# Optimization experiments

Measured on AMD Instinct MI355X. Metric: run time of the kernel, lower is better.

## Reference

```python
import jax, jax.numpy as jnp
import numpy as np
from jax import lax

K_NEIGH = 10


def setup_inputs() -> dict:
    key = jax.random.key(0)
    k1, k2, k3, k4, k5 = jax.random.split(key, 5)
    bs, C, T = 8, 256, 2048
    x = jax.random.normal(k1, (bs, C, T), dtype=jnp.float32)
    num_frms = jax.random.randint(k2, (bs,), 0, 2048)
    # Conv1d(in=C, out=C, kernel=3, pad=1): weight [out, in, k], bias [out]
    conv_w = jax.random.normal(k3, (C, C, 3), dtype=jnp.float32) * (1.0 / np.sqrt(3 * C))
    conv_b = jnp.zeros((C,), dtype=jnp.float32)
    # Linear(2*C -> C): weight [out, 2*in], bias [out]
    mlp_w = jax.random.normal(k4, (C, 2 * C), dtype=jnp.float32) * (1.0 / np.sqrt(2 * C))
    mlp_b = jax.random.normal(k5, (C,), dtype=jnp.float32) * 0.01
    return {"x": x, "num_frms": num_frms, "conv_w": conv_w, "conv_b": conv_b,
            "mlp_w": mlp_w, "mlp_b": mlp_b}


def _knn_idx(x, k):
    # x: [bs, C, T]; dif[b,i,j] = ||x[b,:,i] - x[b,:,j]||^2 via norm expansion
    sq = jnp.sum(x * x, axis=1)                      # [bs, T]
    gram = jnp.einsum('bci,bcj->bij', x, x)          # [bs, T, T]
    dif = sq[:, :, None] + sq[:, None, :] - 2.0 * gram
    _, idx = lax.top_k(-dif, k)                      # k smallest distances
    return idx                                       # [bs, T, k]


def reference(x, num_frms, conv_w, conv_b, mlp_w, mlp_b):
    bs, C, T = x.shape
    Cout = conv_w.shape[0]
    # temporal conv branch (kernel 3, stride 1, pad 1)
    c_out = lax.conv_general_dilated(
        x, conv_w, window_strides=(1,), padding=((1, 1),),
        dimension_numbers=('NCH', 'OIH', 'NCH')) + conv_b[None, :, None]
    # graph branch ('par': knn on x)
    idx = _knn_idx(x, K_NEIGH)                                   # [bs, T, k]
    idx_flat = (idx + jnp.arange(bs)[:, None, None] * T).reshape(-1, K_NEIGH)
    feat = x.transpose(0, 2, 1).reshape(bs * T, C)               # [N, C]
    feat_neigh = feat[idx_flat]                                  # [N, k, C]
    ctr = feat[:, None, :]                                       # [N, 1, C]
    cat = jnp.concatenate(
        [feat_neigh, jnp.broadcast_to(ctr, feat_neigh.shape)], axis=-1)  # [N,k,2C]
    g = jnp.einsum('nkc,oc->nko', cat, mlp_w) + mlp_b            # [N, k, Cout]
    # cosine edge weight
    num = jnp.einsum('nkc,nc->nk', feat_neigh, feat)
    den = jnp.sqrt(jnp.sum(feat_neigh * feat_neigh, axis=2)) * \
          jnp.sqrt(jnp.sum(feat * feat, axis=1))[:, None]
    w = num / den                                                # [N, k]
    g = g * w[:, :, None]
    g = jnp.max(g, axis=1)                                       # [N, Cout]
    g_out = g.reshape(bs, T, Cout).transpose(0, 2, 1)            # [bs, Cout, T]
    out = jax.nn.relu(c_out + g_out)
    # MaxPool1d(kernel=2, stride=2)
    out = out.reshape(bs, Cout, T // 2, 2).max(axis=-1)
    return out
```

## Files before the change

kernel.cpp:

```cpp
#include <hip/hip_runtime.h>
#include <hip/hip_bf16.h>
#include <cstdint>

#define T_DIM 2048
#define C_DIM 256
#define BS 8
#define NPTS (BS * T_DIM)
#define KNB 10
#define NCH 16

typedef __bf16 bf16x8 __attribute__((ext_vector_type(8)));
typedef float f32x4 __attribute__((ext_vector_type(4)));
typedef unsigned long long u64;

#define AS1 __attribute__((address_space(1)))
#define AS3 __attribute__((address_space(3)))

__device__ __forceinline__ unsigned short f2bf_rn(float f) {
  unsigned u = __float_as_uint(f);
  unsigned r = (u + 0x7FFFu + ((u >> 16) & 1u)) >> 16;
  return (unsigned short)r;
}
__device__ __forceinline__ float bfbits2f(unsigned short h) {
  return __uint_as_float((unsigned)h << 16);
}
__device__ __forceinline__ __bf16 bfbits(unsigned short h) {
  return __builtin_bit_cast(__bf16, h);
}

__device__ __forceinline__ unsigned key_hi(float sqi, float sqj, float gv) {
  float dif = __fmaf_rn(-2.0f, gv, __fadd_rn(sqi, sqj));
  unsigned u = __float_as_uint(dif);
  return (u & 0x80000000u) ? ~u : (u | 0x80000000u);
}
__device__ __forceinline__ unsigned flip32(float dif) {
  unsigned u = __float_as_uint(dif);
  return (u & 0x80000000u) ? ~u : (u | 0x80000000u);
}

__device__ __forceinline__ void stage_tile(const __bf16* __restrict__ src, size_t row0,
                                           int ld, int k0, __bf16* lds, int w, int l) {
  int kofs = ((l & 7) ^ (l >> 3)) * 8;
  const __bf16* g0 = src + (row0 + (size_t)(l >> 3)) * ld + k0 + kofs;
  __bf16* lbase = lds + (size_t)(w * 4) * 512;
#pragma unroll
  for (int q4 = 0; q4 < 4; ++q4) {
    __builtin_amdgcn_global_load_lds((AS1 void*)(g0 + (size_t)(w * 4 + q4) * 8 * ld),
                                     (AS3 void*)(lbase + q4 * 512), 16, 0, 0);
  }
}

__device__ __forceinline__ void stage_tile_conv(const __bf16* __restrict__ src, int m0,
                                                int k0in, const __bf16* __restrict__ zp,
                                                __bf16* lds, int w, int l) {
  int tap = k0in >> 8;
  int kshift = tap - 1;
  int k0 = k0in & 255;
  int kofs = ((l & 7) ^ (l >> 3)) * 8;
  int mb = m0 & (T_DIM - 1);
#pragma unroll
  for (int q4 = 0; q4 < 4; ++q4) {
    int q = w * 4 + q4;
    int row = q * 8 + (l >> 3);
    int t = mb + row + kshift;
    const __bf16* g = ((unsigned)t < (unsigned)T_DIM)
                          ? (src + (size_t)(m0 + row + kshift) * C_DIM + k0 + kofs)
                          : (zp + kofs);
    __builtin_amdgcn_global_load_lds((AS1 void*)g, (AS3 void*)(lds + q * 512), 16, 0, 0);
  }
}

__device__ __forceinline__ bf16x8 read_frag(const __bf16* lds, int t16, int ks, int l) {
  int row = t16 * 16 + (l & 15);
  int kb = ks * 64 + ((l >> 4) << 4);
  int byte = row * 128 + (kb ^ ((row & 7) << 4));
  return *(const bf16x8*)((const char*)lds + byte);
}

__global__ __launch_bounds__(256) void k_transpose_split(const float* __restrict__ x,
                                                         __bf16* __restrict__ Fh,
                                                         __bf16* __restrict__ Fl) {
  __shared__ float tile[32][33];
  int b = blockIdx.z;
  int t0 = blockIdx.x * 32;
  int c0 = blockIdx.y * 32;
  int tx = threadIdx.x & 31, ty = threadIdx.x >> 5;
  const float* xb = x + (size_t)b * C_DIM * T_DIM;
#pragma unroll
  for (int r = 0; r < 4; ++r) {
    int c = c0 + ty + 8 * r;
    tile[ty + 8 * r][tx] = xb[(size_t)c * T_DIM + t0 + tx];
  }
  __syncthreads();
#pragma unroll
  for (int r = 0; r < 4; ++r) {
    int t = t0 + ty + 8 * r;
    float v = tile[tx][ty + 8 * r];
    unsigned short hb = f2bf_rn(v);
    float lo = v - bfbits2f(hb);
    size_t o = ((size_t)b * T_DIM + t) * C_DIM + c0 + tx;
    Fh[o] = bfbits(hb);
    Fl[o] = bfbits(f2bf_rn(lo));
  }
}

__global__ __launch_bounds__(256) void k_sq(const __bf16* __restrict__ Fh,
                                            const __bf16* __restrict__ Fl,
                                            float* __restrict__ sq) {
  int n = blockIdx.x * 4 + (threadIdx.x >> 6);
  int lane = threadIdx.x & 63;
  ushort4 hv = ((const ushort4*)Fh)[(size_t)n * 64 + lane];
  ushort4 lv = ((const ushort4*)Fl)[(size_t)n * 64 + lane];
  float s = 0.f;
  {
    float v;
    v = bfbits2f(hv.x) + bfbits2f(lv.x); s = fmaf(v, v, s);
    v = bfbits2f(hv.y) + bfbits2f(lv.y); s = fmaf(v, v, s);
    v = bfbits2f(hv.z) + bfbits2f(lv.z); s = fmaf(v, v, s);
    v = bfbits2f(hv.w) + bfbits2f(lv.w); s = fmaf(v, v, s);
  }
#pragma unroll
  for (int d = 1; d < 64; d <<= 1) s += __shfl_xor(s, d, 64);
  if (lane == 0) sq[n] = s;
}

__global__ __launch_bounds__(256) void k_gram_reduce(const __bf16* __restrict__ Fh,
                                                     const __bf16* __restrict__ Fl,
                                                     const float* __restrict__ sq,
                                                     u64* __restrict__ kbuf,
                                                     u64* __restrict__ bbuf) {
  __shared__ __bf16 Bh[128 * 64], Bl[128 * 64];
  __shared__ float sqc[128];

  int ch = blockIdx.x, p = blockIdx.y, b = blockIdx.z;
  size_t base = (size_t)b * T_DIM;
  const float* sqb = sq + base;
  int tid = threadIdx.x, w = tid >> 6, l = tid & 63, g = l >> 4;
  int r0 = p * 64;
  int cand0 = ch * 128;
  int myrow = r0 + w * 16 + (l & 15);
  float sqi = sqb[myrow];
  if (tid < 128) sqc[tid] = sqb[cand0 + tid];

  const __bf16* rowbaseh = Fh + ((size_t)(base + myrow)) * C_DIM + g * 8;
  const __bf16* rowbasel = Fl + ((size_t)(base + myrow)) * C_DIM + g * 8;

  f32x4 acc[8];
#pragma unroll
  for (int j = 0; j < 8; ++j) acc[j] = {0.f, 0.f, 0.f, 0.f};

  for (int k0 = 0; k0 < C_DIM; k0 += 64) {
    stage_tile(Fh, base + cand0, C_DIM, k0, Bh, w, l);
    stage_tile(Fl, base + cand0, C_DIM, k0, Bl, w, l);
    bf16x8 rhf0 = *(const bf16x8*)(rowbaseh + k0);
    bf16x8 rhf1 = *(const bf16x8*)(rowbaseh + k0 + 32);
    bf16x8 rlf0 = *(const bf16x8*)(rowbasel + k0);
    bf16x8 rlf1 = *(const bf16x8*)(rowbasel + k0 + 32);
    __syncthreads();
#pragma unroll
    for (int ks = 0; ks < 2; ++ks) {
      bf16x8 rh = ks ? rhf1 : rhf0;
      bf16x8 rl = ks ? rlf1 : rlf0;
      bf16x8 cv[8];
#pragma unroll
      for (int j = 0; j < 8; ++j) cv[j] = read_frag(Bh, j, ks, l);
#pragma unroll
      for (int j = 0; j < 8; ++j)
        acc[j] = __builtin_amdgcn_mfma_f32_16x16x32_bf16(cv[j], rh, acc[j], 0, 0, 0);
#pragma unroll
      for (int j = 0; j < 8; ++j)
        acc[j] = __builtin_amdgcn_mfma_f32_16x16x32_bf16(cv[j], rl, acc[j], 0, 0, 0);
#pragma unroll
      for (int j = 0; j < 8; ++j) cv[j] = read_frag(Bl, j, ks, l);
#pragma unroll
      for (int j = 0; j < 8; ++j)
        acc[j] = __builtin_amdgcn_mfma_f32_16x16x32_bf16(cv[j], rh, acc[j], 0, 0, 0);
    }
    __syncthreads();
  }

  u64 c0 = ~0ull, c1 = ~0ull, c2 = ~0ull, c3 = ~0ull;
#pragma unroll
  for (int j = 0; j < 8; ++j) {
    f32x4 sv = *(const f32x4*)&sqc[j * 16 + (g << 2)];
#pragma unroll
    for (int r = 0; r < 4; ++r) {
      unsigned u = key_hi(sqi, sv[r], acc[j][r]);
      u64 key = ((u64)u << 32) | (unsigned)(cand0 + j * 16 + (g << 2) + r);
      u64 t1 = (key > c0) ? key : c0; c0 = (key < c0) ? key : c0;
      u64 t2 = (t1 > c1) ? t1 : c1;  c1 = (t1 < c1) ? t1 : c1;
      u64 t3 = (t2 > c2) ? t2 : c2;  c2 = (t2 < c2) ? t2 : c2;
      c3 = (t3 < c3) ? t3 : c3;
    }
  }
  u64* kp = kbuf + ((((size_t)b * NCH + ch) * T_DIM + myrow) * 12 + g * 3);
  kp[0] = c0;
  kp[1] = c1;
  kp[2] = c2;
  u64 bd = c3;
  { u64 o = __shfl_xor(bd, 16, 64); bd = (o < bd) ? o : bd; }
  { u64 o = __shfl_xor(bd, 32, 64); bd = (o < bd) ? o : bd; }
  if (g == 0) bbuf[((size_t)b * NCH + ch) * T_DIM + myrow] = bd;
}

__global__ __launch_bounds__(256) void k_topk_merge(const u64* __restrict__ kbuf,
                                                    const u64* __restrict__ bbuf,
                                                    const float* __restrict__ sq,
                                                    int* __restrict__ idxo,
                                                    float* __restrict__ wo,
                                                    int* __restrict__ fixlist,
                                                    int* __restrict__ fixcount) {
  int b = blockIdx.y;
  int row = blockIdx.x * 4 + (threadIdx.x >> 6);
  int lane = threadIdx.x & 63;
  const float* sqb = sq + (size_t)b * T_DIM;
  float sqi = sqb[row];

  const u64* kp = kbuf + ((((size_t)b * NCH + (lane >> 2)) * T_DIM + row) * 12 + (lane & 3) * 3);
  u64 m0 = kp[0], m1 = kp[1], m2 = kp[2];
  u64 excl = (lane < NCH) ? bbuf[((size_t)b * NCH + lane) * T_DIM + row] : ~0ull;

  u64 win[KNB];
#pragma unroll
  for (int s = 0; s < KNB; ++s) {
    unsigned mh = (unsigned)(m0 >> 32);
    unsigned h = mh;
#pragma unroll
    for (int d = 1; d < 64; d <<= 1) {
      unsigned oh = __shfl_xor(h, d, 64);
      h = (oh < h) ? oh : h;
    }
    unsigned lo = (mh == h) ? (unsigned)m0 : 0xFFFFFFFFu;
#pragma unroll
    for (int d = 1; d < 64; d <<= 1) {
      unsigned ol = __shfl_xor(lo, d, 64);
      lo = (ol < lo) ? ol : lo;
    }
    u64 m = ((u64)h << 32) | lo;
    win[s] = m;
    bool pop = (m0 == m);
    m0 = pop ? m1 : m0;
    m1 = pop ? m2 : m1;
    m2 = pop ? ~0ull : m2;
  }
  u64 theta = win[KNB - 1];

  u64 mywin = win[0];
#pragma unroll
  for (int s = 1; s < KNB; ++s) mywin = (lane == s) ? win[s] : mywin;
  if (lane < KNB) {
    int j = (int)(unsigned)(mywin & 0xffffffffull);
    unsigned su = (unsigned)(mywin >> 32);
    unsigned bits = (su & 0x80000000u) ? (su & 0x7fffffffu) : ~su;
    float dif = __uint_as_float(bits);
    float sqj = sqb[j];
    float num = 0.5f * (sqi + sqj - dif);
    float wv = num / (sqrtf(sqi) * sqrtf(sqj));
    idxo[((size_t)b * T_DIM + row) * KNB + lane] = j;
    wo[((size_t)b * T_DIM + row) * KNB + lane] = wv;
  }

#pragma unroll
  for (int d = 1; d < 64; d <<= 1) {
    u64 o = __shfl_xor(excl, d, 64);
    excl = (o < excl) ? o : excl;
  }
  if (lane == 0 && excl < theta) {
    int slot = atomicAdd(fixcount, 1);
    fixlist[slot] = (int)(b * T_DIM + row);
  }
}

__global__ __launch_bounds__(256) void k_fix_dots(const __bf16* __restrict__ Fh,
                                                  const __bf16* __restrict__ Fl,
                                                  const float* __restrict__ sq,
                                                  const int* __restrict__ fixlist,
                                                  const int* __restrict__ fixcount,
                                                  u64* __restrict__ kpart) {
  __shared__ float xr[C_DIM];
  __shared__ float difs[64];
  int n = fixcount[0];
  int q = blockIdx.x;
  int tid = threadIdx.x;
  const unsigned short* fh = (const unsigned short*)Fh;
  const unsigned short* fl = (const unsigned short*)Fl;
  for (int i = blockIdx.y; i < n; i += gridDim.y) {
    int rowg = fixlist[i];
    int b = rowg >> 11, r = rowg & (T_DIM - 1);
    xr[tid] = bfbits2f(fh[(size_t)rowg * C_DIM + tid]) + bfbits2f(fl[(size_t)rowg * C_DIM + tid]);
    __syncthreads();
    const float* sqb = sq + (size_t)b * T_DIM;
    float sqi = sqb[r];
    int cand = q * 64 + (tid >> 2);
    int qd = tid & 3;
    size_t jo = ((size_t)b * T_DIM + cand) * C_DIM + qd * 64;
    float p = 0.f;
#pragma unroll 4
    for (int k = 0; k < 16; ++k) {
      ushort4 h4 = *(const ushort4*)(fh + jo + k * 4);
      ushort4 l4 = *(const ushort4*)(fl + jo + k * 4);
      int xb_ = qd * 64 + k * 4;
      p = fmaf(bfbits2f(h4.x) + bfbits2f(l4.x), xr[xb_ + 0], p);
      p = fmaf(bfbits2f(h4.y) + bfbits2f(l4.y), xr[xb_ + 1], p);
      p = fmaf(bfbits2f(h4.z) + bfbits2f(l4.z), xr[xb_ + 2], p);
      p = fmaf(bfbits2f(h4.w) + bfbits2f(l4.w), xr[xb_ + 3], p);
    }
    p += __shfl_xor(p, 1, 64);
    p += __shfl_xor(p, 2, 64);
    if (qd == 0) difs[tid >> 2] = __fmaf_rn(-2.0f, p, __fadd_rn(sqi, sqb[cand]));
    __syncthreads();
    if (tid < 64) {
      int lane = tid;
      u64 key = ((u64)flip32(difs[lane]) << 32) | (unsigned)(q * 64 + lane);
      u64 mywin = ~0ull;
#pragma unroll
      for (int s = 0; s < KNB; ++s) {
        u64 m = key;
#pragma unroll
        for (int d = 1; d < 64; d <<= 1) {
          u64 o = __shfl_xor(m, d, 64);
          m = (o < m) ? o : m;
        }
        if (key == m) key = ~0ull;
        mywin = (lane == s) ? m : mywin;
      }
      if (lane < KNB) kpart[((size_t)i * 32 + q) * KNB + lane] = mywin;
    }
    __syncthreads();
  }
}

__global__ __launch_bounds__(256) void k_fix_merge(const float* __restrict__ sq,
                                                   const int* __restrict__ fixlist,
                                                   const int* __restrict__ fixcount,
                                                   const u64* __restrict__ kpart,
                                                   int* __restrict__ idxo,
                                                   float* __restrict__ wo) {
  int n = fixcount[0];
  int w = threadIdx.x >> 6, lane = threadIdx.x & 63;
  for (int i = blockIdx.x * 4 + w; i < n; i += gridDim.x * 4) {
    int rowg = fixlist[i];
    int b = rowg >> 11, r = rowg & (T_DIM - 1);
    const float* sqb = sq + (size_t)b * T_DIM;
    float sqi = sqb[r];
    const u64* kp = kpart + (size_t)i * 320;
    u64 s0 = kp[lane], s1 = ~0ull, s2 = ~0ull, s3 = ~0ull, s4 = ~0ull;
#pragma unroll
    for (int t = 1; t < 5; ++t) {
      u64 k = kp[lane + 64 * t];
      u64 hi;
      hi = (k > s0) ? k : s0; s0 = (k < s0) ? k : s0; k = hi;
      hi = (k > s1) ? k : s1; s1 = (k < s1) ? k : s1; k = hi;
      hi = (k > s2) ? k : s2; s2 = (k < s2) ? k : s2; k = hi;
      hi = (k > s3) ? k : s3; s3 = (k < s3) ? k : s3; k = hi;
      s4 = (k < s4) ? k : s4;
    }
    u64 mywin = ~0ull;
#pragma unroll
    for (int s = 0; s < KNB; ++s) {
      u64 m = s0;
#pragma unroll
      for (int d = 1; d < 64; d <<= 1) {
        u64 o = __shfl_xor(m, d, 64);
        m = (o < m) ? o : m;
      }
      bool pop = (s0 == m);
      s0 = pop ? s1 : s0; s1 = pop ? s2 : s1; s2 = pop ? s3 : s2;
      s3 = pop ? s4 : s3; s4 = pop ? ~0ull : s4;
      mywin = (lane == s) ? m : mywin;
    }
    if (lane < KNB) {
      int j = (int)(unsigned)(mywin & 0xffffffffull);
      unsigned su = (unsigned)(mywin >> 32);
      unsigned bits = (su & 0x80000000u) ? (su & 0x7fffffffu) : ~su;
      float dif = __uint_as_float(bits);
      float sqj = sqb[j];
      float num = 0.5f * (sqi + sqj - dif);
      float wv = num / (sqrtf(sqi) * sqrtf(sqj));
      idxo[((size_t)b * T_DIM + r) * KNB + lane] = j;
      wo[((size_t)b * T_DIM + r) * KNB + lane] = wv;
    }
  }
}

__global__ __launch_bounds__(256, 2) void k_gemm_fused(const __bf16* __restrict__ Fh,
                                                       const __bf16* __restrict__ mlpB,
                                                       const __bf16* __restrict__ wk3,
                                                       float* __restrict__ mlpout,
                                                       float* __restrict__ convout,
                                                       const __bf16* __restrict__ zp) {
  __shared__ __bf16 As[128 * 64], Bs[128 * 64];
  int bx = blockIdx.x;
  const __bf16* Bm;
  float* C;
  int N, K, conv, n0;
  if (bx < 4) {
    Bm = mlpB; C = mlpout; N = 512; K = 256; conv = 0; n0 = bx * 128;
  } else {
    Bm = wk3; C = convout; N = 256; K = 768; conv = 1; n0 = (bx - 4) * 128;
  }
  int m0 = blockIdx.y * 128;
  int tid = threadIdx.x, w = tid >> 6, l = tid & 63;
  int wr = w >> 1, wc = w & 1;
  f32x4 acc[4][4];
#pragma unroll
  for (int i = 0; i < 4; ++i)
#pragma unroll
    for (int j = 0; j < 4; ++j) acc[i][j] = {0.f, 0.f, 0.f, 0.f};

  for (int k0 = 0; k0 < K; k0 += 64) {
    if (conv)
      stage_tile_conv(Fh, m0, k0, zp, As, w, l);
    else
      stage_tile(Fh, (size_t)m0, C_DIM, k0, As, w, l);
    stage_tile(Bm, (size_t)n0, K, k0, Bs, w, l);
    __syncthreads();
#pragma unroll
    for (int ks = 0; ks < 2; ++ks) {
      bf16x8 af[4], bf_[4];
#pragma unroll
      for (int i = 0; i < 4; ++i) af[i] = read_frag(As, wr * 4 + i, ks, l);
#pragma unroll
      for (int j = 0; j < 4; ++j) bf_[j] = read_frag(Bs, wc * 4 + j, ks, l);
#pragma unroll
      for (int i = 0; i < 4; ++i)
#pragma unroll
        for (int j = 0; j < 4; ++j)
          acc[i][j] = __builtin_amdgcn_mfma_f32_16x16x32_bf16(af[i], bf_[j], acc[i][j], 0, 0, 0);
    }
    __syncthreads();
  }
#pragma unroll
  for (int i = 0; i < 4; ++i) {
    int mrow = m0 + wr * 64 + i * 16 + ((l >> 4) << 2);
#pragma unroll
    for (int j = 0; j < 4; ++j) {
      int ncol = n0 + wc * 64 + j * 16 + (l & 15);
      float* cp = C + (size_t)mrow * N + ncol;
#pragma unroll
      for (int r = 0; r < 4; ++r) cp[(size_t)r * N] = acc[i][j][r];
    }
  }
}

__global__ __launch_bounds__(256) void k_gfinal(const float* __restrict__ mlpout,
                                                const float* __restrict__ mlp_b,
                                                const int* __restrict__ idxo,
                                                const float* __restrict__ wo,
                                                const float* __restrict__ convb,
                                                const float* __restrict__ cb,
                                                float* __restrict__ out) {
  __shared__ float tile[32][33];
  __shared__ int sj[64][KNB];
  __shared__ float sw[64][KNB];
  int b = blockIdx.z, c0 = blockIdx.y * 32, t20 = blockIdx.x * 32;
  int tid = threadIdx.x;
  int nbase = b * T_DIM + t20 * 2;
  for (int e = tid; e < 64 * KNB; e += 256) {
    int ln = e / KNB, k = e - ln * KNB;
    sj[ln][k] = b * T_DIM + idxo[(size_t)(nbase + ln) * KNB + k];
    sw[ln][k] = wo[(size_t)(nbase + ln) * KNB + k];
  }
  __syncthreads();
  int tx = tid & 31, ty = tid >> 5;
  int c = c0 + tx;
  float bias_c = cb[c];
  float mbias = mlp_b[c];
#pragma unroll
  for (int rr = 0; rr < 4; ++rr) {
    int lt2 = ty + 8 * rr;
    float res[2];
#pragma unroll
    for (int s = 0; s < 2; ++s) {
      int ln = 2 * lt2 + s;
      int n = nbase + ln;
      float q = mlpout[(size_t)n * 512 + 256 + c] + mbias;
      float mx = -3.4e38f;
#pragma unroll
      for (int k = 0; k < KNB; ++k) {
        float v = (mlpout[(size_t)sj[ln][k] * 512 + c] + q) * sw[ln][k];
        mx = fmaxf(mx, v);
      }
      float v = convb[(size_t)n * C_DIM + c] + mx + bias_c;
      res[s] = fmaxf(v, 0.f);
    }
    tile[lt2][tx] = fmaxf(res[0], res[1]);
  }
  __syncthreads();
#pragma unroll
  for (int rr = 0; rr < 4; ++rr) {
    int cc = c0 + ty + 8 * rr;
    out[((size_t)b * C_DIM + cc) * (T_DIM / 2) + t20 + tx] = tile[tx][ty + 8 * rr];
  }
}

__global__ void k_repack(const float* __restrict__ cw, const float* __restrict__ mw,
                         __bf16* __restrict__ wk3, __bf16* __restrict__ mlpB,
                         __bf16* __restrict__ zp, int* __restrict__ fixcount) {
  int i = blockIdx.x * 256 + threadIdx.x;
  if (i == 0) fixcount[0] = 0;
  if (i < 3 * C_DIM * C_DIM) {
    int o = i / 768;
    int rem = i - o * 768;
    int tap = rem >> 8;
    int ii = rem & 255;
    wk3[i] = bfbits(f2bf_rn(cw[(size_t)o * 768 + ii * 3 + tap]));
  } else {
    int m = i - 3 * C_DIM * C_DIM;
    if (m < 512 * 256) {
      int r = m >> 8;
      int col = m & 255;
      mlpB[m] = bfbits(f2bf_rn(mw[(size_t)(r & 255) * 512 + ((r >> 8) << 8) + col]));
    }
  }
  if (blockIdx.x == 0 && threadIdx.x < 128) zp[threadIdx.x] = bfbits(0);
}

extern "C" void kernel_launch(void* const* d_in, const int* in_sizes, int n_in,
                              void* d_out, int out_size, void* d_ws, size_t ws_size,
                              hipStream_t stream) {
  const float* x = (const float*)d_in[0];
  const float* conv_w = (const float*)d_in[2];
  const float* conv_b = (const float*)d_in[3];
  const float* mlp_w = (const float*)d_in[4];
  const float* mlp_b = (const float*)d_in[5];
  float* out = (float*)d_out;

  char* ws = (char*)d_ws;
  size_t off = 0;
  auto alloc = [&](size_t bytes) -> void* {
    void* p = ws + off;
    off += (bytes + 255) & ~(size_t)255;
    return p;
  };
  __bf16* Fh = (__bf16*)alloc((size_t)NPTS * C_DIM * 2);
  __bf16* Fl = (__bf16*)alloc((size_t)NPTS * C_DIM * 2);
  float* convout = (float*)alloc((size_t)NPTS * C_DIM * 4);
  float* mlpout = (float*)alloc((size_t)NPTS * 512 * 4);
  float* sq = (float*)alloc((size_t)NPTS * 4);
  int* idxb = (int*)alloc((size_t)NPTS * KNB * 4);
  float* wb = (float*)alloc((size_t)NPTS * KNB * 4);
  int* fixlist = (int*)alloc((size_t)NPTS * 4);
  int* fixcount = (int*)alloc(256);
  u64* kbuf = (u64*)alloc((size_t)BS * NCH * T_DIM * 12 * 8);
  u64* bbuf = (u64*)alloc((size_t)BS * NCH * T_DIM * 8);
  u64* kpart = (u64*)alloc((size_t)NPTS * 32 * KNB * 8);
  __bf16* wk3 = (__bf16*)alloc((size_t)3 * C_DIM * C_DIM * 2);
  __bf16* mlpB = (__bf16*)alloc((size_t)512 * 256 * 2);
  __bf16* zp = (__bf16*)alloc(512);

  k_repack<<<dim3(1280), 256, 0, stream>>>(conv_w, mlp_w, wk3, mlpB, zp, fixcount);
  k_transpose_split<<<dim3(T_DIM / 32, C_DIM / 32, BS), 256, 0, stream>>>(x, Fh, Fl);
  k_sq<<<dim3(NPTS / 4), 256, 0, stream>>>(Fh, Fl, sq);

  k_gram_reduce<<<dim3(NCH, T_DIM / 64, BS), 256, 0, stream>>>(Fh, Fl, sq, kbuf, bbuf);
  k_topk_merge<<<dim3(T_DIM / 4, BS), 256, 0, stream>>>(kbuf, bbuf, sq, idxb, wb, fixlist, fixcount);
  k_fix_dots<<<dim3(32, 64), 256, 0, stream>>>(Fh, Fl, sq, fixlist, fixcount, kpart);
  k_fix_merge<<<dim3(64), 256, 0, stream>>>(sq, fixlist, fixcount, kpart, idxb, wb);

  k_gemm_fused<<<dim3(6, NPTS / 128), 256, 0, stream>>>(Fh, mlpB, wk3, mlpout, convout, zp);

  k_gfinal<<<dim3((T_DIM / 2) / 32, C_DIM / 32, BS), 256, 0, stream>>>(
      mlpout, mlp_b, idxb, wb, convout, conv_b, out);
}
```

Measured before the change: 171.5 us.

## Exploit Gram matrix symmetry by computing only upper-triangular 128x128 tiles

Replaces the full Gram+partial-top-k kernel with one that computes only the 136 upper-triangular 128x128 tiles per batch. Each tile is used twice: rows against candidates directly from registers, and the transposed view through a 64KB shared-memory staging buffer. This roughly halves the MFMA work and the global loads for the distance matrix. In exchange it uses more LDS per block, which lowers occupancy, adds transpose reads from shared memory, and produces a smaller grid of larger blocks. On diagonal tiles both passes write the same kbuf slots, which is harmless because they hold the same result.

```diff
diff --git a/kernel.cpp b/kernel.cpp
--- a/kernel.cpp
+++ b/kernel.cpp
@@ -124,83 +124,133 @@
   if (lane == 0) sq[n] = s;
 }
 
-__global__ __launch_bounds__(256) void k_gram_reduce(const __bf16* __restrict__ Fh,
-                                                     const __bf16* __restrict__ Fl,
-                                                     const float* __restrict__ sq,
-                                                     u64* __restrict__ kbuf,
-                                                     u64* __restrict__ bbuf) {
-  __shared__ __bf16 Bh[128 * 64], Bl[128 * 64];
-  __shared__ float sqc[128];
-
-  int ch = blockIdx.x, p = blockIdx.y, b = blockIdx.z;
+__global__ __launch_bounds__(256) void k_gram_sym_reduce(const __bf16* __restrict__ Fh,
+                                                         const __bf16* __restrict__ Fl,
+                                                         const float* __restrict__ sq,
+                                                         u64* __restrict__ kbuf,
+                                                         u64* __restrict__ bbuf) {
+  __shared__ __align__(16) char smem[65536];
+  __bf16* Bh = (__bf16*)smem;
+  __bf16* Bl = (__bf16*)(smem + 16384);
+  __bf16* Rh = (__bf16*)(smem + 32768);
+  __bf16* Rl = (__bf16*)(smem + 49152);
+  float* T2 = (float*)smem;
+
+  int ti = blockIdx.x, b = blockIdx.y;
+  int cx = (int)((sqrtf(8.0f * (float)ti + 1.0f) - 1.0f) * 0.5f);
+  if ((cx + 1) * (cx + 2) / 2 <= ti) cx++;
+  int py = ti - cx * (cx + 1) / 2;
+
   size_t base = (size_t)b * T_DIM;
   const float* sqb = sq + base;
+  int cand0 = cx * 128, row0 = py * 128;
   int tid = threadIdx.x, w = tid >> 6, l = tid & 63, g = l >> 4;
-  int r0 = p * 64;
-  int cand0 = ch * 128;
-  int myrow = r0 + w * 16 + (l & 15);
-  float sqi = sqb[myrow];
-  if (tid < 128) sqc[tid] = sqb[cand0 + tid];
-
-  const __bf16* rowbaseh = Fh + ((size_t)(base + myrow)) * C_DIM + g * 8;
-  const __bf16* rowbasel = Fl + ((size_t)(base + myrow)) * C_DIM + g * 8;
-
-  f32x4 acc[8];
-#pragma unroll
-  for (int j = 0; j < 8; ++j) acc[j] = {0.f, 0.f, 0.f, 0.f};
+
+  f32x4 acc[8][2];
+#pragma unroll
+  for (int j = 0; j < 8; ++j) {
+    acc[j][0] = {0.f, 0.f, 0.f, 0.f};
+    acc[j][1] = {0.f, 0.f, 0.f, 0.f};
+  }
 
   for (int k0 = 0; k0 < C_DIM; k0 += 64) {
     stage_tile(Fh, base + cand0, C_DIM, k0, Bh, w, l);
     stage_tile(Fl, base + cand0, C_DIM, k0, Bl, w, l);
-    bf16x8 rhf0 = *(const bf16x8*)(rowbaseh + k0);
-    bf16x8 rhf1 = *(const bf16x8*)(rowbaseh + k0 + 32);
-    bf16x8 rlf0 = *(const bf16x8*)(rowbasel + k0);
-    bf16x8 rlf1 = *(const bf16x8*)(rowbasel + k0 + 32);
+    stage_tile(Fh, base + row0, C_DIM, k0, Rh, w, l);
+    stage_tile(Fl, base + row0, C_DIM, k0, Rl, w, l);
     __syncthreads();
 #pragma unroll
     for (int ks = 0; ks < 2; ++ks) {
-      bf16x8 rh = ks ? rhf1 : rhf0;
-      bf16x8 rl = ks ? rlf1 : rlf0;
+      bf16x8 rh0 = read_frag(Rh, w * 2 + 0, ks, l);
+      bf16x8 rh1 = read_frag(Rh, w * 2 + 1, ks, l);
+      bf16x8 rl0 = read_frag(Rl, w * 2 + 0, ks, l);
+      bf16x8 rl1 = read_frag(Rl, w * 2 + 1, ks, l);
       bf16x8 cv[8];
 #pragma unroll
       for (int j = 0; j < 8; ++j) cv[j] = read_frag(Bh, j, ks, l);
 #pragma unroll
-      for (int j = 0; j < 8; ++j)
-        acc[j] = __builtin_amdgcn_mfma_f32_16x16x32_bf16(cv[j], rh, acc[j], 0, 0, 0);
-#pragma unroll
-      for (int j = 0; j < 8; ++j)
-        acc[j] = __builtin_amdgcn_mfma_f32_16x16x32_bf16(cv[j], rl, acc[j], 0, 0, 0);
+      for (int j = 0; j < 8; ++j) {
+        acc[j][0] = __builtin_amdgcn_mfma_f32_16x16x32_bf16(cv[j], rh0, acc[j][0], 0, 0, 0);
+        acc[j][1] = __builtin_amdgcn_mfma_f32_16x16x32_bf16(cv[j], rh1, acc[j][1], 0, 0, 0);
+      }
+#pragma unroll
+      for (int j = 0; j < 8; ++j) {
+        acc[j][0] = __builtin_amdgcn_mfma_f32_16x16x32_bf16(cv[j], rl0, acc[j][0], 0, 0, 0);
+        acc[j][1] = __builtin_amdgcn_mfma_f32_16x16x32_bf16(cv[j], rl1, acc[j][1], 0, 0, 0);
+      }
 #pragma unroll
       for (int j = 0; j < 8; ++j) cv[j] = read_frag(Bl, j, ks, l);
 #pragma unroll
-      for (int j = 0; j < 8; ++j)
-        acc[j] = __builtin_amdgcn_mfma_f32_16x16x32_bf16(cv[j], rh, acc[j], 0, 0, 0);
+      for (int j = 0; j < 8; ++j) {
+        acc[j][0] = __builtin_amdgcn_mfma_f32_16x16x32_bf16(cv[j], rh0, acc[j][0], 0, 0, 0);
+        acc[j][1] = __builtin_amdgcn_mfma_f32_16x16x32_bf16(cv[j], rh1, acc[j][1], 0, 0, 0);
+      }
     }
     __syncthreads();
   }
 
-  u64 c0 = ~0ull, c1 = ~0ull, c2 = ~0ull, c3 = ~0ull;
-#pragma unroll
-  for (int j = 0; j < 8; ++j) {
-    f32x4 sv = *(const f32x4*)&sqc[j * 16 + (g << 2)];
-#pragma unroll
-    for (int r = 0; r < 4; ++r) {
-      unsigned u = key_hi(sqi, sv[r], acc[j][r]);
-      u64 key = ((u64)u << 32) | (unsigned)(cand0 + j * 16 + (g << 2) + r);
-      u64 t1 = (key > c0) ? key : c0; c0 = (key < c0) ? key : c0;
-      u64 t2 = (t1 > c1) ? t1 : c1;  c1 = (t1 < c1) ? t1 : c1;
-      u64 t3 = (t2 > c2) ? t2 : c2;  c2 = (t2 < c2) ? t2 : c2;
-      c3 = (t3 < c3) ? t3 : c3;
-    }
-  }
-  u64* kp = kbuf + ((((size_t)b * NCH + ch) * T_DIM + myrow) * 12 + g * 3);
-  kp[0] = c0;
-  kp[1] = c1;
-  kp[2] = c2;
-  u64 bd = c3;
-  { u64 o = __shfl_xor(bd, 16, 64); bd = (o < bd) ? o : bd; }
-  { u64 o = __shfl_xor(bd, 32, 64); bd = (o < bd) ? o : bd; }
-  if (g == 0) bbuf[((size_t)b * NCH + ch) * T_DIM + myrow] = bd;
+#pragma unroll
+  for (int jr = 0; jr < 2; ++jr) {
+    int rl_ = w * 32 + jr * 16 + (l & 15);
+#pragma unroll
+    for (int j = 0; j < 8; ++j)
+      *(f32x4*)&T2[(size_t)rl_ * 128 + j * 16 + (g << 2)] = acc[j][jr];
+  }
+
+#pragma unroll
+  for (int jr = 0; jr < 2; ++jr) {
+    int rl_ = w * 32 + jr * 16 + (l & 15);
+    float sqi = sqb[row0 + rl_];
+    u64 c0 = ~0ull, c1 = ~0ull, c2 = ~0ull, c3 = ~0ull;
+#pragma unroll
+    for (int j = 0; j < 8; ++j) {
+      f32x4 sv = *(const f32x4*)&sqb[cand0 + j * 16 + (g << 2)];
+#pragma unroll
+      for (int r = 0; r < 4; ++r) {
+        unsigned u = key_hi(sqi, sv[r], acc[j][jr][r]);
+        u64 key = ((u64)u << 32) | (unsigned)(cand0 + j * 16 + (g << 2) + r);
+        u64 t1 = (key > c0) ? key : c0; c0 = (key < c0) ? key : c0;
+        u64 t2 = (t1 > c1) ? t1 : c1;  c1 = (t1 < c1) ? t1 : c1;
+        u64 t3 = (t2 > c2) ? t2 : c2;  c2 = (t2 < c2) ? t2 : c2;
+        c3 = (t3 < c3) ? t3 : c3;
+      }
+    }
+    u64* kp = kbuf + ((((size_t)b * NCH + cx) * T_DIM + row0 + rl_) * 12 + g * 3);
+    kp[0] = c0; kp[1] = c1; kp[2] = c2;
+    u64 bd = c3;
+    { u64 o = __shfl_xor(bd, 16, 64); bd = (o < bd) ? o : bd; }
+    { u64 o = __shfl_xor(bd, 32, 64); bd = (o < bd) ? o : bd; }
+    if (g == 0) bbuf[((size_t)b * NCH + cx) * T_DIM + row0 + rl_] = bd;
+  }
+
+  __syncthreads();
+
+#pragma unroll
+  for (int jrm = 0; jrm < 2; ++jrm) {
+    int cl_ = w * 32 + jrm * 16 + (l & 15);
+    float sqi = sqb[cand0 + cl_];
+    u64 c0 = ~0ull, c1 = ~0ull, c2 = ~0ull, c3 = ~0ull;
+#pragma unroll
+    for (int j = 0; j < 8; ++j) {
+      f32x4 sv = *(const f32x4*)&sqb[row0 + j * 16 + (g << 2)];
+#pragma unroll
+      for (int r = 0; r < 4; ++r) {
+        float score = T2[(size_t)(j * 16 + (g << 2) + r) * 128 + cl_];
+        unsigned u = key_hi(sqi, sv[r], score);
+        u64 key = ((u64)u << 32) | (unsigned)(row0 + j * 16 + (g << 2) + r);
+        u64 t1 = (key > c0) ? key : c0; c0 = (key < c0) ? key : c0;
+        u64 t2 = (t1 > c1) ? t1 : c1;  c1 = (t1 < c1) ? t1 : c1;
+        u64 t3 = (t2 > c2) ? t2 : c2;  c2 = (t2 < c2) ? t2 : c2;
+        c3 = (t3 < c3) ? t3 : c3;
+      }
+    }
+    u64* kp = kbuf + ((((size_t)b * NCH + py) * T_DIM + cand0 + cl_) * 12 + g * 3);
+    kp[0] = c0; kp[1] = c1; kp[2] = c2;
+    u64 bd = c3;
+    { u64 o = __shfl_xor(bd, 16, 64); bd = (o < bd) ? o : bd; }
+    { u64 o = __shfl_xor(bd, 32, 64); bd = (o < bd) ? o : bd; }
+    if (g == 0) bbuf[((size_t)b * NCH + py) * T_DIM + cand0 + cl_] = bd;
+  }
 }
 
 __global__ __launch_bounds__(256) void k_topk_merge(const u64* __restrict__ kbuf,
@@ -553,7 +603,7 @@
   k_transpose_split<<<dim3(T_DIM / 32, C_DIM / 32, BS), 256, 0, stream>>>(x, Fh, Fl);
   k_sq<<<dim3(NPTS / 4), 256, 0, stream>>>(Fh, Fl, sq);
 
-  k_gram_reduce<<<dim3(NCH, T_DIM / 64, BS), 256, 0, stream>>>(Fh, Fl, sq, kbuf, bbuf);
+  k_gram_sym_reduce<<<dim3(136, BS), 256, 0, stream>>>(Fh, Fl, sq, kbuf, bbuf);
   k_topk_merge<<<dim3(T_DIM / 4, BS), 256, 0, stream>>>(kbuf, bbuf, sq, idxb, wb, fixlist, fixcount);
   k_fix_dots<<<dim3(32, 64), 256, 0, stream>>>(Fh, Fl, sq, fixlist, fixcount, kpart);
   k_fix_merge<<<dim3(64), 256, 0, stream>>>(sq, fixlist, fixcount, kpart, idxb, wb);
```

Measured after the change: 172.2 us. Within noise of the previous version (+0.4%).

## Enlarge gram tile to 128 rows staged in LDS with two row fragments per wave

Applied to the files above, without the earlier changes.

The gram/top-k kernel now processes 128 query rows per block instead of 64. Row operands are staged into shared memory alongside the candidate tile, and each wave computes two 16-row fragments, so every candidate fragment read from LDS is reused twice. This halves the grid and the redundant candidate staging per row. In exchange it doubles accumulator registers and LDS use, which may lower occupancy. The squared norms are now read directly from global memory instead of a shared cache.

```diff
diff --git a/kernel.cpp b/kernel.cpp
--- a/kernel.cpp
+++ b/kernel.cpp
@@ -130,77 +130,85 @@
                                                      u64* __restrict__ kbuf,
                                                      u64* __restrict__ bbuf) {
   __shared__ __bf16 Bh[128 * 64], Bl[128 * 64];
-  __shared__ float sqc[128];
+  __shared__ __bf16 Rh[128 * 64], Rl[128 * 64];
 
   int ch = blockIdx.x, p = blockIdx.y, b = blockIdx.z;
   size_t base = (size_t)b * T_DIM;
   const float* sqb = sq + base;
   int tid = threadIdx.x, w = tid >> 6, l = tid & 63, g = l >> 4;
-  int r0 = p * 64;
+  int r0 = p * 128;
   int cand0 = ch * 128;
-  int myrow = r0 + w * 16 + (l & 15);
-  float sqi = sqb[myrow];
-  if (tid < 128) sqc[tid] = sqb[cand0 + tid];
-
-  const __bf16* rowbaseh = Fh + ((size_t)(base + myrow)) * C_DIM + g * 8;
-  const __bf16* rowbasel = Fl + ((size_t)(base + myrow)) * C_DIM + g * 8;
-
-  f32x4 acc[8];
-#pragma unroll
-  for (int j = 0; j < 8; ++j) acc[j] = {0.f, 0.f, 0.f, 0.f};
+
+  f32x4 acc[8][2];
+#pragma unroll
+  for (int j = 0; j < 8; ++j) {
+    acc[j][0] = {0.f, 0.f, 0.f, 0.f};
+    acc[j][1] = {0.f, 0.f, 0.f, 0.f};
+  }
 
   for (int k0 = 0; k0 < C_DIM; k0 += 64) {
     stage_tile(Fh, base + cand0, C_DIM, k0, Bh, w, l);
     stage_tile(Fl, base + cand0, C_DIM, k0, Bl, w, l);
-    bf16x8 rhf0 = *(const bf16x8*)(rowbaseh + k0);
-    bf16x8 rhf1 = *(const bf16x8*)(rowbaseh + k0 + 32);
-    bf16x8 rlf0 = *(const bf16x8*)(rowbasel + k0);
-    bf16x8 rlf1 = *(const bf16x8*)(rowbasel + k0 + 32);
+    stage_tile(Fh, base + r0, C_DIM, k0, Rh, w, l);
+    stage_tile(Fl, base + r0, C_DIM, k0, Rl, w, l);
     __syncthreads();
 #pragma unroll
     for (int ks = 0; ks < 2; ++ks) {
-      bf16x8 rh = ks ? rhf1 : rhf0;
-      bf16x8 rl = ks ? rlf1 : rlf0;
+      bf16x8 rh0 = read_frag(Rh, w * 2 + 0, ks, l);
+      bf16x8 rh1 = read_frag(Rh, w * 2 + 1, ks, l);
+      bf16x8 rl0 = read_frag(Rl, w * 2 + 0, ks, l);
+      bf16x8 rl1 = read_frag(Rl, w * 2 + 1, ks, l);
       bf16x8 cv[8];
 #pragma unroll
       for (int j = 0; j < 8; ++j) cv[j] = read_frag(Bh, j, ks, l);
 #pragma unroll
-      for (int j = 0; j < 8; ++j)
-        acc[j] = __builtin_amdgcn_mfma_f32_16x16x32_bf16(cv[j], rh, acc[j], 0, 0, 0);
-#pragma unroll
-      for (int j = 0; j < 8; ++j)
-        acc[j] = __builtin_amdgcn_mfma_f32_16x16x32_bf16(cv[j], rl, acc[j], 0, 0, 0);
+      for (int j = 0; j < 8; ++j) {
+        acc[j][0] = __builtin_amdgcn_mfma_f32_16x16x32_bf16(cv[j], rh0, acc[j][0], 0, 0, 0);
+        acc[j][1] = __builtin_amdgcn_mfma_f32_16x16x32_bf16(cv[j], rh1, acc[j][1], 0, 0, 0);
+      }
+#pragma unroll
+      for (int j = 0; j < 8; ++j) {
+        acc[j][0] = __builtin_amdgcn_mfma_f32_16x16x32_bf16(cv[j], rl0, acc[j][0], 0, 0, 0);
+        acc[j][1] = __builtin_amdgcn_mfma_f32_16x16x32_bf16(cv[j], rl1, acc[j][1], 0, 0, 0);
+      }
 #pragma unroll
       for (int j = 0; j < 8; ++j) cv[j] = read_frag(Bl, j, ks, l);
 #pragma unroll
-      for (int j = 0; j < 8; ++j)
-        acc[j] = __builtin_amdgcn_mfma_f32_16x16x32_bf16(cv[j], rh, acc[j], 0, 0, 0);
-    }
-    __syncthreads();
-  }
-
-  u64 c0 = ~0ull, c1 = ~0ull, c2 = ~0ull, c3 = ~0ull;
-#pragma unroll
-  for (int j = 0; j < 8; ++j) {
-    f32x4 sv = *(const f32x4*)&sqc[j * 16 + (g << 2)];
-#pragma unroll
-    for (int r = 0; r < 4; ++r) {
-      unsigned u = key_hi(sqi, sv[r], acc[j][r]);
-      u64 key = ((u64)u << 32) | (unsigned)(cand0 + j * 16 + (g << 2) + r);
-      u64 t1 = (key > c0) ? key : c0; c0 = (key < c0) ? key : c0;
-      u64 t2 = (t1 > c1) ? t1 : c1;  c1 = (t1 < c1) ? t1 : c1;
-      u64 t3 = (t2 > c2) ? t2 : c2;  c2 = (t2 < c2) ? t2 : c2;
-      c3 = (t3 < c3) ? t3 : c3;
-    }
-  }
-  u64* kp = kbuf + ((((size_t)b * NCH + ch) * T_DIM + myrow) * 12 + g * 3);
-  kp[0] = c0;
-  kp[1] = c1;
-  kp[2] = c2;
-  u64 bd = c3;
-  { u64 o = __shfl_xor(bd, 16, 64); bd = (o < bd) ? o : bd; }
-  { u64 o = __shfl_xor(bd, 32, 64); bd = (o < bd) ? o : bd; }
-  if (g == 0) bbuf[((size_t)b * NCH + ch) * T_DIM + myrow] = bd;
+      for (int j = 0; j < 8; ++j) {
+        acc[j][0] = __builtin_amdgcn_mfma_f32_16x16x32_bf16(cv[j], rh0, acc[j][0], 0, 0, 0);
+        acc[j][1] = __builtin_amdgcn_mfma_f32_16x16x32_bf16(cv[j], rh1, acc[j][1], 0, 0, 0);
+      }
+    }
+    __syncthreads();
+  }
+
+#pragma unroll
+  for (int jr = 0; jr < 2; ++jr) {
+    int myrow = r0 + w * 32 + jr * 16 + (l & 15);
+    float sqi = sqb[myrow];
+    u64 c0 = ~0ull, c1 = ~0ull, c2 = ~0ull, c3 = ~0ull;
+#pragma unroll
+    for (int j = 0; j < 8; ++j) {
+      f32x4 sv = *(const f32x4*)&sqb[cand0 + j * 16 + (g << 2)];
+#pragma unroll
+      for (int r = 0; r < 4; ++r) {
+        unsigned u = key_hi(sqi, sv[r], acc[j][jr][r]);
+        u64 key = ((u64)u << 32) | (unsigned)(cand0 + j * 16 + (g << 2) + r);
+        u64 t1 = (key > c0) ? key : c0; c0 = (key < c0) ? key : c0;
+        u64 t2 = (t1 > c1) ? t1 : c1;  c1 = (t1 < c1) ? t1 : c1;
+        u64 t3 = (t2 > c2) ? t2 : c2;  c2 = (t2 < c2) ? t2 : c2;
+        c3 = (t3 < c3) ? t3 : c3;
+      }
+    }
+    u64* kp = kbuf + ((((size_t)b * NCH + ch) * T_DIM + myrow) * 12 + g * 3);
+    kp[0] = c0;
+    kp[1] = c1;
+    kp[2] = c2;
+    u64 bd = c3;
+    { u64 o = __shfl_xor(bd, 16, 64); bd = (o < bd) ? o : bd; }
+    { u64 o = __shfl_xor(bd, 32, 64); bd = (o < bd) ? o : bd; }
+    if (g == 0) bbuf[((size_t)b * NCH + ch) * T_DIM + myrow] = bd;
+  }
 }
 
 __global__ __launch_bounds__(256) void k_topk_merge(const u64* __restrict__ kbuf,
@@ -553,7 +561,7 @@
   k_transpose_split<<<dim3(T_DIM / 32, C_DIM / 32, BS), 256, 0, stream>>>(x, Fh, Fl);
   k_sq<<<dim3(NPTS / 4), 256, 0, stream>>>(Fh, Fl, sq);
 
-  k_gram_reduce<<<dim3(NCH, T_DIM / 64, BS), 256, 0, stream>>>(Fh, Fl, sq, kbuf, bbuf);
+  k_gram_reduce<<<dim3(NCH, T_DIM / 128, BS), 256, 0, stream>>>(Fh, Fl, sq, kbuf, bbuf);
   k_topk_merge<<<dim3(T_DIM / 4, BS), 256, 0, stream>>>(kbuf, bbuf, sq, idxb, wb, fixlist, fixcount);
   k_fix_dots<<<dim3(32, 64), 256, 0, stream>>>(Fh, Fl, sq, fixlist, fixcount, kpart);
   k_fix_merge<<<dim3(64), 256, 0, stream>>>(sq, fixlist, fixcount, kpart, idxb, wb);
```

Measured after the change: 169.2 us. No clear change (-1.4%).
